# Performance work log

Measured on AMD Instinct MI355X. Metric: run time of the kernel, lower is better.

The kernel has to match this reference:

```python
import jax, jax.numpy as jnp
import numpy as np

B, N, C, D = 4, 4096, 1024, 32  # batch, tokens, channels, head dim
EPS = 1e-15
PAD_VAL = 1.0


def setup_inputs() -> dict:
    key = jax.random.key(0)
    k1, k2, k3 = jax.random.split(key, 3)
    x = jax.random.normal(k1, (B, N, C), dtype=jnp.float32)
    W_qkv = jax.random.normal(k2, (3 * C, C), dtype=jnp.float32) * 0.02
    W_proj = jax.random.normal(k3, (C, C), dtype=jnp.float32) * 0.02
    b_proj = jnp.zeros((C,), dtype=jnp.float32)
    return {"x": x, "W_qkv": W_qkv, "W_proj": W_proj, "b_proj": b_proj}


def reference(x, W_qkv, W_proj, b_proj):
    Bx, Nx, Cx = x.shape
    h = Cx // D
    # qkv projection (no bias), then split as torch: reshape(B,N,3,C).permute(0,2,3,1)
    qkv = jnp.einsum('bnc,oc->bno', x, W_qkv)            # [B,N,3C]
    qkv = qkv.reshape(Bx, Nx, 3, Cx).transpose(0, 2, 3, 1)  # [B,3,C,N]
    q, k, v = qkv[:, 0], qkv[:, 1], qkv[:, 2]
    q = jax.nn.relu(q.reshape(Bx, h, D, Nx))             # [B,h,D,N]
    k = jax.nn.relu(k.reshape(Bx, h, D, Nx)).transpose(0, 1, 3, 2)  # [B,h,N,D]
    v = v.reshape(Bx, h, D, Nx)                          # [B,h,D,N]
    # pad v with a row of PAD_VAL=1 to carry the normalizer
    v = jnp.concatenate([v, jnp.full((Bx, h, 1, Nx), PAD_VAL, v.dtype)], axis=2)  # [B,h,D+1,N]
    vk = jnp.einsum('bhdn,bhne->bhde', v, k)             # [B,h,D+1,D]
    out = jnp.einsum('bhde,bhen->bhdn', vk, q)           # [B,h,D+1,N]
    out = out[:, :, :-1] / (out[:, :, -1:] + EPS)        # [B,h,D,N]
    out = out.reshape(Bx, Cx, Nx).transpose(0, 2, 1)     # [B,N,C]
    return jnp.einsum('bnc,oc->bno', out, W_proj) + b_proj
```

## Files before the change

kernel.cpp:

```cpp
#include <hip/hip_runtime.h>


using us8   = __attribute__((ext_vector_type(8))) unsigned short;
using us4   = __attribute__((ext_vector_type(4))) unsigned short;
using s8v   = __attribute__((ext_vector_type(8))) short;
using f32x4 = __attribute__((ext_vector_type(4))) float;

__device__ __forceinline__ unsigned short f2bf(float f) {
    union { float f; unsigned int u; } c; c.f = f;
    unsigned int r = c.u + 0x7fffu + ((c.u >> 16) & 1u);
    return (unsigned short)(r >> 16);
}
__device__ __forceinline__ float bf2f(unsigned short u) {
    union { unsigned int u; float f; } c; c.u = ((unsigned int)u) << 16;
    return c.f;
}

__device__ __forceinline__ void async16(const unsigned short* g, unsigned short* l) {
    __builtin_amdgcn_global_load_lds(
        (const __attribute__((address_space(1))) unsigned int*)g,
        (__attribute__((address_space(3))) unsigned int*)l, 16, 0, 0);
}

__global__ __launch_bounds__(256)
void prep(const float* __restrict__ x, const float* __restrict__ wq,
          const float* __restrict__ wp, unsigned short* __restrict__ xb,
          unsigned short* __restrict__ wqb, unsigned short* __restrict__ wpb,
          float* __restrict__ vkws) {
    const int NX = 16777216 / 8, NQ = 3145728 / 8, NP = 1048576 / 8, NZ = 135168 / 8;
    int gid = blockIdx.x * 256 + threadIdx.x;
    const float* in; unsigned short* out; int i;
    if (gid < NX)                    { in = x;  out = xb;  i = gid * 8; }
    else if (gid < NX + NQ)          { in = wq; out = wqb; i = (gid - NX) * 8; }
    else if (gid < NX + NQ + NP)     { in = wp; out = wpb; i = (gid - NX - NQ) * 8; }
    else if (gid < NX + NQ + NP + NZ) {
        int z = (gid - NX - NQ - NP) * 8;
        f32x4 zero = {};
        *(f32x4*)(vkws + z) = zero; *(f32x4*)(vkws + z + 4) = zero;
        return;
    } else return;
    float4 a = *(const float4*)(in + i);
    float4 b = *(const float4*)(in + i + 4);
    us8 o;
    o[0] = f2bf(a.x); o[1] = f2bf(a.y); o[2] = f2bf(a.z); o[3] = f2bf(a.w);
    o[4] = f2bf(b.x); o[5] = f2bf(b.y); o[6] = f2bf(b.z); o[7] = f2bf(b.w);
    *(us8*)(out + i) = o;
}

#define FENCE() asm volatile("" ::: "memory")
#define BARX()  do { FENCE(); __builtin_amdgcn_s_barrier(); FENCE(); } while (0)

#define MFMA_H(AF, BF, MB)                                                   \
  do {                                                                       \
    __builtin_amdgcn_s_setprio(1);                                           \
    _Pragma("unroll")                                                        \
    for (int mi_ = 0; mi_ < 4; ++mi_)                                        \
      _Pragma("unroll")                                                      \
      for (int ni_ = 0; ni_ < 4; ++ni_)                                      \
        _Pragma("unroll")                                                    \
        for (int kk_ = 0; kk_ < 2; ++kk_)                                    \
          acc[(MB) + mi_][ni_] = __builtin_amdgcn_mfma_f32_16x16x32_bf16(    \
              AF[mi_][kk_], BF[ni_][kk_], acc[(MB) + mi_][ni_], 0, 0, 0);    \
    __builtin_amdgcn_s_setprio(0);                                           \
  } while (0)

#define GATHERB(DST, KT)                                                     \
  do {                                                                       \
    _Pragma("unroll")                                                        \
    for (int ni_ = 0; ni_ < 4; ++ni_) {                                      \
      DST[ni_][0] = *(const s8v*)(Bgl + (size_t)ni_ * 16384 + (KT));         \
      DST[ni_][1] = *(const s8v*)(Bgl + (size_t)ni_ * 16384 + (KT) + 32);    \
    }                                                                        \
  } while (0)

#define STAGEA(KT, BUF)                                                      \
  do {                                                                       \
    _Pragma("unroll")                                                        \
    for (int j_ = 0; j_ < 4; ++j_)                                           \
      async16(Aglane + (size_t)j_ * 65536 + (KT),                            \
              (BUF) + j_ * 4096 + wv * 512);                                 \
  } while (0)

#define TILEG(G, BUSE, BPRE)                                                 \
  do {                                                                       \
    unsigned short* bufR = lds + 16384 * ((G) % 3);                          \
    unsigned short* bufS = lds + 16384 * (((G) + 2) % 3);                    \
    const int ktB = ((G) + 1 < 16 ? (G) + 1 : 15) * 64;                      \
    const int ktA = ((G) + 2 < 16 ? (G) + 2 : 15) * 64;                      \
    _Pragma("unroll")                                                        \
    for (int mi_ = 0; mi_ < 4; ++mi_) {                                      \
      af[mi_][0] = *(const s8v*)&bufR[(wr * 128 + mi_ * 16 + mrow) * 64 + ks0]; \
      af[mi_][1] = *(const s8v*)&bufR[(wr * 128 + mi_ * 16 + mrow) * 64 + ks1]; \
    }                                                                        \
    GATHERB(BPRE, ktB);                                                      \
    FENCE();                                                                 \
    MFMA_H(af, BUSE, 0);                                                     \
    STAGEA(ktA, bufS);                                                       \
    FENCE();                                                                 \
    _Pragma("unroll")                                                        \
    for (int mi_ = 0; mi_ < 4; ++mi_) {                                      \
      af[mi_][0] = *(const s8v*)&bufR[(wr * 128 + 64 + mi_ * 16 + mrow) * 64 + ks0]; \
      af[mi_][1] = *(const s8v*)&bufR[(wr * 128 + 64 + mi_ * 16 + mrow) * 64 + ks1]; \
    }                                                                        \
    MFMA_H(af, BUSE, 4);                                                     \
    asm volatile("s_waitcnt vmcnt(12)" ::: "memory");                        \
    BARX();                                                                  \
  } while (0)

template <int MODE>
__device__ __forceinline__
void gemm_core256(const unsigned short* __restrict__ A,
                  const unsigned short* __restrict__ Bt,
                  unsigned short* __restrict__ Cq,
                  unsigned short* __restrict__ kvT,
                  float* __restrict__ Cf, const float* __restrict__ bias,
                  int N, int tM, int tN, unsigned short* lds) {
    const int t    = threadIdx.x;
    const int lane = t & 63;
    const int wv   = t >> 6;
    const int wr   = wv >> 2;
    const int wc   = wv & 3;
    const int mrow = lane & 15;
    const int kq   = lane >> 4;
    const int m7   = lane & 7;

    const int row0 = t >> 3;
    const int esw  = ((t & 7) ^ (row0 & 7)) * 8;
    const unsigned short* Aglane = A + (size_t)(tM + row0) * 1024 + esw;

    const unsigned short* Bgl =
        Bt + (size_t)(tN + wc * 64 + mrow) * 1024 + kq * 8;

    const int ks0 = ((0 * 4 + kq) ^ m7) * 8;
    const int ks1 = ((1 * 4 + kq) ^ m7) * 8;

    f32x4 acc[8][4] = {};
    s8v af[4][2], bA[4][2], bB[4][2];

    STAGEA(0, lds);
    STAGEA(64, lds + 16384);
    FENCE();
    GATHERB(bA, 0);
    asm volatile("s_waitcnt vmcnt(12)" ::: "memory");
    BARX();

#pragma unroll
    for (int g2 = 0; g2 < 8; ++g2) {
        TILEG(2 * g2,     bA, bB);
        TILEG(2 * g2 + 1, bB, bA);
    }

    const int crow0 = kq * 4;
    const int ccol  = mrow;
    if (MODE == 0) {
        if (tN >= 1024) {
            const int b2  = tM >> 12;
            const int nb0 = (tM & 4095) + wr * 128;
#pragma unroll
            for (int mi = 0; mi < 8; ++mi) {
                const int nbase = nb0 + mi * 16 + crow0;
#pragma unroll
                for (int ni = 0; ni < 4; ++ni) {
                    const int col = tN + wc * 64 + ni * 16 + ccol;
                    f32x4 v = acc[mi][ni];
                    if (col < 2048) {
                        v[0] = fmaxf(v[0], 0.f); v[1] = fmaxf(v[1], 0.f);
                        v[2] = fmaxf(v[2], 0.f); v[3] = fmaxf(v[3], 0.f);
                    }
                    us4 o;
                    o[0] = f2bf(v[0]); o[1] = f2bf(v[1]);
                    o[2] = f2bf(v[2]); o[3] = f2bf(v[3]);
                    *(us4*)&kvT[((size_t)b2 * 2048 + (col - 1024)) * 4096 + nbase] = o;
                }
            }
        } else {
#pragma unroll
            for (int mi = 0; mi < 8; ++mi)
#pragma unroll
                for (int ni = 0; ni < 4; ++ni) {
                    const int row = tM + wr * 128 + mi * 16 + crow0;
                    const int col = tN + wc * 64 + ni * 16 + ccol;
#pragma unroll
                    for (int r2 = 0; r2 < 4; ++r2)
                        Cq[(size_t)(row + r2) * 1024 + col] =
                            f2bf(fmaxf(acc[mi][ni][r2], 0.f));
                }
        }
    } else {
#pragma unroll
        for (int mi = 0; mi < 8; ++mi)
#pragma unroll
            for (int ni = 0; ni < 4; ++ni) {
                const int row = tM + wr * 128 + mi * 16 + crow0;
                const int col = tN + wc * 64 + ni * 16 + ccol;
#pragma unroll
                for (int r2 = 0; r2 < 4; ++r2)
                    Cf[(size_t)(row + r2) * N + col] = acc[mi][ni][r2] + bias[col];
            }
    }
    asm volatile("s_waitcnt vmcnt(0)" ::: "memory");
}

__device__ __forceinline__ void xcd_map256(int blk, int MT, int& tM, int& tN) {
    const int xcd = blk & 7;
    const int i   = blk >> 3;
    const int MTx = MT >> 3;
    const int ppan = MTx * 4;
    const int p   = i / ppan;
    const int i2  = i % ppan;
    tM = (xcd * MTx + (i2 >> 2)) * 256;
    tN = (p * 4 + (i2 & 3)) * 256;
}

__global__ __launch_bounds__(512, 2)
void gemm_qkv(const unsigned short* __restrict__ A,
              const unsigned short* __restrict__ Bt,
              unsigned short* __restrict__ Cq, unsigned short* __restrict__ kvT,
              int M, int N) {
    extern __shared__ unsigned short lds[];
    int tM, tN;
    xcd_map256(blockIdx.x, M >> 8, tM, tN);
    gemm_core256<0>(A, Bt, Cq, kvT, nullptr, nullptr, N, tM, tN, lds);
}

__global__ __launch_bounds__(512, 2)
void gemm_proj(const unsigned short* __restrict__ A,
               const unsigned short* __restrict__ Bt,
               float* __restrict__ C, const float* __restrict__ bias,
               int M, int N) {
    extern __shared__ unsigned short lds[];
    int tM, tN;
    xcd_map256(blockIdx.x, M >> 8, tM, tN);
    gemm_core256<1>(A, Bt, nullptr, nullptr, C, bias, N, tM, tN, lds);
}

__global__ __launch_bounds__(256)
void lite_vk(const unsigned short* __restrict__ kvT, float* __restrict__ vkws) {
    const int bh = blockIdx.x, ck = blockIdx.y;
    const int b = bh >> 5, h = bh & 31;
    const int S = 136;
    __shared__ unsigned short Ks[32 * S];
    __shared__ unsigned short Vs[32 * S];
    __shared__ float Rs[4][1088];
    const int t = threadIdx.x, lane = t & 63, wv = t >> 6;
    const unsigned short* Kp = kvT + ((size_t)b * 2048 + h * 32) * 4096 + ck * 512;
    const unsigned short* Vp = kvT + ((size_t)b * 2048 + 1024 + h * 32) * 4096 + ck * 512;
    const int sr = t >> 3, ss = (t & 7) * 16;
    f32x4 acc00 = {}, acc01 = {}, acc10 = {}, acc11 = {}, accO0 = {}, accO1 = {};
    s8v ones;
#pragma unroll
    for (int j = 0; j < 8; ++j) ones[j] = (short)0x3F80;
    const int mrow = lane & 15, kq = (lane >> 4) * 8;

    for (int tile = 0; tile < 4; ++tile) {
        int go = tile * 128 + ss;
        us8 k0v = *(const us8*)(Kp + (size_t)sr * 4096 + go);
        us8 k1v = *(const us8*)(Kp + (size_t)sr * 4096 + go + 8);
        us8 v0v = *(const us8*)(Vp + (size_t)sr * 4096 + go);
        us8 v1v = *(const us8*)(Vp + (size_t)sr * 4096 + go + 8);
        __syncthreads();
        *(us8*)&Ks[sr * S + ss]     = k0v;
        *(us8*)&Ks[sr * S + ss + 8] = k1v;
        *(us8*)&Vs[sr * S + ss]     = v0v;
        *(us8*)&Vs[sr * S + ss + 8] = v1v;
        __syncthreads();
        int ko = wv * 32 + kq;
        s8v a0 = *(const s8v*)&Vs[(mrow)      * S + ko];
        s8v a1 = *(const s8v*)&Vs[(16 + mrow) * S + ko];
        s8v b0 = *(const s8v*)&Ks[(mrow)      * S + ko];
        s8v b1 = *(const s8v*)&Ks[(16 + mrow) * S + ko];
        acc00 = __builtin_amdgcn_mfma_f32_16x16x32_bf16(a0, b0, acc00, 0, 0, 0);
        acc01 = __builtin_amdgcn_mfma_f32_16x16x32_bf16(a0, b1, acc01, 0, 0, 0);
        acc10 = __builtin_amdgcn_mfma_f32_16x16x32_bf16(a1, b0, acc10, 0, 0, 0);
        acc11 = __builtin_amdgcn_mfma_f32_16x16x32_bf16(a1, b1, acc11, 0, 0, 0);
        accO0 = __builtin_amdgcn_mfma_f32_16x16x32_bf16(ones, b0, accO0, 0, 0, 0);
        accO1 = __builtin_amdgcn_mfma_f32_16x16x32_bf16(ones, b1, accO1, 0, 0, 0);
    }

    const int ccol = lane & 15, crow = (lane >> 4) * 4;
    float* R = Rs[wv];
#pragma unroll
    for (int r2 = 0; r2 < 4; ++r2) {
        R[(crow + r2) * 32 + ccol]           = acc00[r2];
        R[(crow + r2) * 32 + 16 + ccol]      = acc01[r2];
        R[(16 + crow + r2) * 32 + ccol]      = acc10[r2];
        R[(16 + crow + r2) * 32 + 16 + ccol] = acc11[r2];
    }
    if ((lane >> 4) == 0) {
        R[1024 + ccol]      = accO0[0];
        R[1024 + 16 + ccol] = accO1[0];
    }
    __syncthreads();
    float* vkb = vkws + bh * (33 * 32);
    for (int i = t; i < 1056; i += 256) {
        float s = Rs[0][i] + Rs[1][i] + Rs[2][i] + Rs[3][i];
        atomicAdd(&vkb[i], s);
    }
}

__global__ __launch_bounds__(256)
void lite_apply(const unsigned short* __restrict__ qb,
                const float* __restrict__ vkws,
                unsigned short* __restrict__ yb) {
    const int bh = blockIdx.x, nb = blockIdx.y;
    const int b = bh >> 5, h = bh & 31;
    __shared__ unsigned short vkh[48 * 32];
    __shared__ unsigned short vkl[48 * 32];
    const int t = threadIdx.x;
    for (int i = t; i < 48 * 32; i += 256) {
        float v = (i < 33 * 32) ? vkws[bh * (33 * 32) + i] : 0.f;
        unsigned short hi = f2bf(v);
        vkh[i] = hi;
        vkl[i] = f2bf(v - bf2f(hi));
    }
    __syncthreads();

    const int lane = t & 63, wv = t >> 6;
    const int col = lane & 15, quad = lane >> 4;
    s8v b0h = *(const s8v*)&vkh[(col)      * 32 + quad * 8];
    s8v b0l = *(const s8v*)&vkl[(col)      * 32 + quad * 8];
    s8v b1h = *(const s8v*)&vkh[(16 + col) * 32 + quad * 8];
    s8v b1l = *(const s8v*)&vkl[(16 + col) * 32 + quad * 8];
    s8v b2h = *(const s8v*)&vkh[(32 + col) * 32 + quad * 8];
    s8v b2l = *(const s8v*)&vkl[(32 + col) * 32 + quad * 8];

    const int ntile = nb * 256 + wv * 64;
#pragma unroll
    for (int mi = 0; mi < 4; ++mi) {
        int tok = ntile + mi * 16 + col;
        const unsigned short* qp =
            qb + (size_t)(b * 4096 + tok) * 1024 + h * 32 + quad * 8;
        s8v a = *(const s8v*)qp;
        f32x4 n0 = {}, n1 = {}, dd = {};
        n0 = __builtin_amdgcn_mfma_f32_16x16x32_bf16(b0h, a, n0, 0, 0, 0);
        n0 = __builtin_amdgcn_mfma_f32_16x16x32_bf16(b0l, a, n0, 0, 0, 0);
        n1 = __builtin_amdgcn_mfma_f32_16x16x32_bf16(b1h, a, n1, 0, 0, 0);
        n1 = __builtin_amdgcn_mfma_f32_16x16x32_bf16(b1l, a, n1, 0, 0, 0);
        dd = __builtin_amdgcn_mfma_f32_16x16x32_bf16(b2h, a, dd, 0, 0, 0);
        dd = __builtin_amdgcn_mfma_f32_16x16x32_bf16(b2l, a, dd, 0, 0, 0);
        float den  = __shfl(dd[0], col, 64);
        float rinv = 1.f / (den + 1e-15f);
        us4 o0, o1;
#pragma unroll
        for (int r = 0; r < 4; ++r) {
            o0[r] = f2bf(n0[r] * rinv);
            o1[r] = f2bf(n1[r] * rinv);
        }
        size_t o = (size_t)(b * 4096 + tok) * 1024 + h * 32;
        *(us4*)&yb[o + quad * 4]      = o0;
        *(us4*)&yb[o + 16 + quad * 4] = o1;
    }
}

extern "C" void kernel_launch(void* const* d_in, const int* in_sizes, int n_in,
                              void* d_out, int out_size, void* d_ws, size_t ws_size,
                              hipStream_t stream) {
    const float* x     = (const float*)d_in[0];
    const float* Wqkv  = (const float*)d_in[1];
    const float* Wproj = (const float*)d_in[2];
    const float* bproj = (const float*)d_in[3];
    float* out = (float*)d_out;

    const int M = 16384, Cdim = 1024, O1 = 3072;

    unsigned short* xb     = (unsigned short*)d_ws;
    unsigned short* wqkvb  = xb + (size_t)M * Cdim;
    unsigned short* wprojb = wqkvb + (size_t)O1 * Cdim;
    unsigned short* qb     = wprojb + (size_t)Cdim * Cdim;
    unsigned short* kvT    = qb + (size_t)M * Cdim;
    unsigned short* ybuf   = kvT + (size_t)4 * 2048 * 4096;
    float* vkws            = (float*)(ybuf + (size_t)M * Cdim);

    static int attr_done = 0;
    if (!attr_done) {
        hipFuncSetAttribute((const void*)gemm_qkv,
                            hipFuncAttributeMaxDynamicSharedMemorySize, 98304);
        hipFuncSetAttribute((const void*)gemm_proj,
                            hipFuncAttributeMaxDynamicSharedMemorySize, 98304);
        attr_done = 1;
    }

    const int PREP_GROUPS = (16777216 + 3145728 + 1048576 + 135168) / 8;
    prep<<<(PREP_GROUPS + 255) / 256, 256, 0, stream>>>(
        x, Wqkv, Wproj, xb, wqkvb, wprojb, vkws);

    gemm_qkv<<<(M / 256) * (O1 / 256), 512, 98304, stream>>>(
        xb, wqkvb, qb, kvT, M, O1);

    lite_vk<<<dim3(128, 8), 256, 0, stream>>>(kvT, vkws);
    lite_apply<<<dim3(128, 16), 256, 0, stream>>>(qb, vkws, ybuf);

    gemm_proj<<<(M / 256) * (Cdim / 256), 512, 98304, stream>>>(
        ybuf, wprojb, out, bproj, M, Cdim);
}
```

Measured before the change: 358.3 us.

## Stage both A and B tiles through LDS with 32-wide K steps

Replaces the GEMM main loop, which staged only A through a three-buffer LDS ring (64-wide K) and gathered B straight from global memory into registers. Both A and B are now loaded asynchronously into LDS with a new XOR swizzle and K step 32, giving a 32-iteration rotating triple-buffer loop. The goal is coalesced, shared B loads instead of per-wave scattered global reads. In exchange there are twice as many barriers per K, less unrolling, and more LDS traffic per MFMA.

```diff
diff --git a/kernel.cpp b/kernel.cpp
--- a/kernel.cpp
+++ b/kernel.cpp
@@ -47,64 +47,17 @@
     *(us8*)(out + i) = o;
 }
 
+constexpr int TSZ = 16384;
+
 #define FENCE() asm volatile("" ::: "memory")
 #define BARX()  do { FENCE(); __builtin_amdgcn_s_barrier(); FENCE(); } while (0)
 
-#define MFMA_H(AF, BF, MB)                                                   \
+#define STAGE(KT, BS)                                                        \
   do {                                                                       \
-    __builtin_amdgcn_s_setprio(1);                                           \
-    _Pragma("unroll")                                                        \
-    for (int mi_ = 0; mi_ < 4; ++mi_)                                        \
-      _Pragma("unroll")                                                      \
-      for (int ni_ = 0; ni_ < 4; ++ni_)                                      \
-        _Pragma("unroll")                                                    \
-        for (int kk_ = 0; kk_ < 2; ++kk_)                                    \
-          acc[(MB) + mi_][ni_] = __builtin_amdgcn_mfma_f32_16x16x32_bf16(    \
-              AF[mi_][kk_], BF[ni_][kk_], acc[(MB) + mi_][ni_], 0, 0, 0);    \
-    __builtin_amdgcn_s_setprio(0);                                           \
-  } while (0)
-
-#define GATHERB(DST, KT)                                                     \
-  do {                                                                       \
-    _Pragma("unroll")                                                        \
-    for (int ni_ = 0; ni_ < 4; ++ni_) {                                      \
-      DST[ni_][0] = *(const s8v*)(Bgl + (size_t)ni_ * 16384 + (KT));         \
-      DST[ni_][1] = *(const s8v*)(Bgl + (size_t)ni_ * 16384 + (KT) + 32);    \
-    }                                                                        \
-  } while (0)
-
-#define STAGEA(KT, BUF)                                                      \
-  do {                                                                       \
-    _Pragma("unroll")                                                        \
-    for (int j_ = 0; j_ < 4; ++j_)                                           \
-      async16(Aglane + (size_t)j_ * 65536 + (KT),                            \
-              (BUF) + j_ * 4096 + wv * 512);                                 \
-  } while (0)
-
-#define TILEG(G, BUSE, BPRE)                                                 \
-  do {                                                                       \
-    unsigned short* bufR = lds + 16384 * ((G) % 3);                          \
-    unsigned short* bufS = lds + 16384 * (((G) + 2) % 3);                    \
-    const int ktB = ((G) + 1 < 16 ? (G) + 1 : 15) * 64;                      \
-    const int ktA = ((G) + 2 < 16 ? (G) + 2 : 15) * 64;                      \
-    _Pragma("unroll")                                                        \
-    for (int mi_ = 0; mi_ < 4; ++mi_) {                                      \
-      af[mi_][0] = *(const s8v*)&bufR[(wr * 128 + mi_ * 16 + mrow) * 64 + ks0]; \
-      af[mi_][1] = *(const s8v*)&bufR[(wr * 128 + mi_ * 16 + mrow) * 64 + ks1]; \
-    }                                                                        \
-    GATHERB(BPRE, ktB);                                                      \
-    FENCE();                                                                 \
-    MFMA_H(af, BUSE, 0);                                                     \
-    STAGEA(ktA, bufS);                                                       \
-    FENCE();                                                                 \
-    _Pragma("unroll")                                                        \
-    for (int mi_ = 0; mi_ < 4; ++mi_) {                                      \
-      af[mi_][0] = *(const s8v*)&bufR[(wr * 128 + 64 + mi_ * 16 + mrow) * 64 + ks0]; \
-      af[mi_][1] = *(const s8v*)&bufR[(wr * 128 + 64 + mi_ * 16 + mrow) * 64 + ks1]; \
-    }                                                                        \
-    MFMA_H(af, BUSE, 4);                                                     \
-    asm volatile("s_waitcnt vmcnt(12)" ::: "memory");                        \
-    BARX();                                                                  \
+    async16(Ag + g0 + (KT), (BS) + d0);                                      \
+    async16(Ag + g1 + (KT), (BS) + d1);                                      \
+    async16(Bg + g0 + (KT), (BS) + 8192 + d0);                               \
+    async16(Bg + g1 + (KT), (BS) + 8192 + d1);                               \
   } while (0)
 
 template <int MODE>
@@ -122,32 +75,53 @@
     const int wc   = wv & 3;
     const int mrow = lane & 15;
     const int kq   = lane >> 4;
-    const int m7   = lane & 7;
-
-    const int row0 = t >> 3;
-    const int esw  = ((t & 7) ^ (row0 & 7)) * 8;
-    const unsigned short* Aglane = A + (size_t)(tM + row0) * 1024 + esw;
-
-    const unsigned short* Bgl =
-        Bt + (size_t)(tN + wc * 64 + mrow) * 1024 + kq * 8;
-
-    const int ks0 = ((0 * 4 + kq) ^ m7) * 8;
-    const int ks1 = ((1 * 4 + kq) ^ m7) * 8;
+
+    const int c0 = t, c1 = 512 + t;
+    const int r0 = c0 >> 2, r1 = c1 >> 2;
+    const int g0 = r0 * 1024 + ((c0 & 3) ^ ((r0 >> 1) & 3)) * 8;
+    const int g1 = r1 * 1024 + ((c1 & 3) ^ ((r1 >> 1) & 3)) * 8;
+    const unsigned short* Ag = A  + (size_t)tM * 1024;
+    const unsigned short* Bg = Bt + (size_t)tN * 1024;
+    const int d0 = wv * 512, d1 = 4096 + wv * 512;
+
+    const int swz  = (kq ^ ((mrow >> 1) & 3)) * 8;
+    const int aoff = (wr * 128 + mrow) * 32 + swz;
+    const int boff = (wc * 64  + mrow) * 32 + swz;
 
     f32x4 acc[8][4] = {};
-    s8v af[4][2], bA[4][2], bB[4][2];
-
-    STAGEA(0, lds);
-    STAGEA(64, lds + 16384);
-    FENCE();
-    GATHERB(bA, 0);
-    asm volatile("s_waitcnt vmcnt(12)" ::: "memory");
+    s8v af[8], bf[4];
+
+    constexpr int NT = 32;
+
+    STAGE(0,  lds);
+    STAGE(32, lds + TSZ);
+    asm volatile("s_waitcnt vmcnt(4)" ::: "memory");
     BARX();
 
-#pragma unroll
-    for (int g2 = 0; g2 < 8; ++g2) {
-        TILEG(2 * g2,     bA, bB);
-        TILEG(2 * g2 + 1, bB, bA);
+    unsigned short* bR = lds;
+    unsigned short* bT = lds + TSZ;
+    unsigned short* bS = lds + 2 * TSZ;
+
+    for (int g = 0; g < NT; ++g) {
+        const int kt = (g + 2 < NT ? g + 2 : NT - 1) * 32;
+#pragma unroll
+        for (int mi = 0; mi < 8; ++mi)
+            af[mi] = *(const s8v*)&bR[aoff + mi * 512];
+#pragma unroll
+        for (int ni = 0; ni < 4; ++ni)
+            bf[ni] = *(const s8v*)&bR[8192 + boff + ni * 512];
+        STAGE(kt, bS);
+        __builtin_amdgcn_s_setprio(1);
+#pragma unroll
+        for (int mi = 0; mi < 8; ++mi)
+#pragma unroll
+            for (int ni = 0; ni < 4; ++ni)
+                acc[mi][ni] = __builtin_amdgcn_mfma_f32_16x16x32_bf16(
+                    af[mi], bf[ni], acc[mi][ni], 0, 0, 0);
+        __builtin_amdgcn_s_setprio(0);
+        asm volatile("s_waitcnt vmcnt(4)" ::: "memory");
+        BARX();
+        unsigned short* tmp = bR; bR = bT; bT = bS; bS = tmp;
     }
 
     const int crow0 = kq * 4;
```

Measured after the change: 314.7 us. 1.14x faster.
